# Kernel optimization log

Hardware: AMD Instinct MI355X
Metric: run time of the kernel (lower is better)

## Reference

```python
import jax, jax.numpy as jnp
import numpy as np

N = 8192
IN_CH = 256
OUT_CH = 64
LEAKY_ALPHA = 0.5
NEG_INF = -9e15  # -9000000000000000.0 from the source


def setup_inputs() -> dict:
    key = jax.random.key(0)
    k1, k2, k3, k4 = jax.random.split(key, 4)
    h = jax.random.normal(k1, (N, IN_CH), dtype=jnp.float32)
    adj = jax.random.randint(k2, (N, N), 0, 2, dtype=jnp.int32)
    # Xavier-uniform-style init for parameters
    limW = float(np.sqrt(6.0 / (IN_CH + OUT_CH)))
    W = jax.random.uniform(k3, (IN_CH, OUT_CH), dtype=jnp.float32, minval=-limW, maxval=limW)
    lima = float(np.sqrt(6.0 / (2 * OUT_CH + 1)))
    a = jax.random.uniform(k4, (2 * OUT_CH, 1), dtype=jnp.float32, minval=-lima, maxval=lima)
    return {"h": h, "adj": adj, "W": W, "a": a}


def reference(h, adj, W, a):
    # Wh: [N, out]
    Wh = h @ W
    # additive attention score: e[i,j] = leakyrelu(Wh[i]@a1 + Wh[j]@a2)
    Wh1 = Wh @ a[:OUT_CH]   # [N, 1]
    Wh2 = Wh @ a[OUT_CH:]   # [N, 1]
    e = Wh1 + Wh2.T         # [N, N]
    e = jnp.where(e >= 0, e, LEAKY_ALPHA * e)  # LeakyReLU(0.5)
    # adjacency masking + row softmax
    att = jnp.where(adj > 0, e, jnp.float32(NEG_INF))
    att = jax.nn.softmax(att, axis=1)
    # dropout is identity in eval mode (training=False)
    h_prime = att @ Wh      # [N, out]
    # concat=True branch applies ReLU on the output
    return jax.nn.relu(h_prime)
```

## Files before the change

### kernel.cpp

```cpp
#include <hip/hip_runtime.h>
#include <stdint.h>

#define NN 8192
#define INC 256
#define OUTC 64
#define LOG2E 1.4426950408889634f

typedef __bf16 bf16x8 __attribute__((ext_vector_type(8)));
typedef float f32x4 __attribute__((ext_vector_type(4)));

__device__ __forceinline__ unsigned short f2bf(float x) {
    union { float f; unsigned u; } v; v.f = x;
    unsigned u = v.u;
    u += 0x7fffu + ((u >> 16) & 1u);
    return (unsigned short)(u >> 16);
}

#if __has_builtin(__builtin_amdgcn_exp2f)
#define EXP2(x) __builtin_amdgcn_exp2f(x)
#else
#define EXP2(x) exp2f(x)
#endif

__global__ __launch_bounds__(256) void gat_k1(
        const float* __restrict__ h, const float* __restrict__ W,
        const float* __restrict__ a,
        unsigned short* __restrict__ WhTf, float* __restrict__ Wh1,
        float* __restrict__ Wh2) {
    __shared__ float Ws[256 * 65];
    __shared__ float hs[16 * INC];
    __shared__ float Wa1s[256], Wa2s[256], as_[128];
    __shared__ unsigned short wt[OUTC][16];
    const int r0 = blockIdx.x * 16;
    const int t  = threadIdx.x;
    if (t < 128) as_[t] = a[t];
    #pragma unroll
    for (int it = 0; it < 16; ++it) {
        int idx = it * 1024 + t * 4;
        float4 v = *reinterpret_cast<const float4*>(W + idx);
        int k = idx >> 6, c = idx & 63;
        float* dst = &Ws[k * 65 + c];
        dst[0] = v.x; dst[1] = v.y; dst[2] = v.z; dst[3] = v.w;
    }
    #pragma unroll
    for (int it = 0; it < 4; ++it) {
        int idx = it * 1024 + t * 4;
        float4 v = *reinterpret_cast<const float4*>(h + (size_t)r0 * INC + idx);
        hs[idx] = v.x; hs[idx + 1] = v.y; hs[idx + 2] = v.z; hs[idx + 3] = v.w;
    }
    __syncthreads();
    {
        float s1 = 0.f, s2 = 0.f;
        #pragma unroll 8
        for (int c = 0; c < OUTC; ++c) {
            float w = Ws[t * 65 + c];
            s1 = fmaf(w, as_[c], s1);
            s2 = fmaf(w, as_[OUTC + c], s2);
        }
        Wa1s[t] = s1; Wa2s[t] = s2;
    }
    __syncthreads();
    const int w = t >> 6, lane = t & 63;
    const int c = lane;
    const float* hr = &hs[w * 4 * INC];
    float acc0 = 0.f, acc1 = 0.f, acc2 = 0.f, acc3 = 0.f;
    #pragma unroll 8
    for (int k = 0; k < INC; ++k) {
        float wv = Ws[k * 65 + c];
        acc0 = fmaf(hr[k],           wv, acc0);
        acc1 = fmaf(hr[INC + k],     wv, acc1);
        acc2 = fmaf(hr[2 * INC + k], wv, acc2);
        acc3 = fmaf(hr[3 * INC + k], wv, acc3);
    }
    float s1r[4] = {0.f, 0.f, 0.f, 0.f}, s2r[4] = {0.f, 0.f, 0.f, 0.f};
    #pragma unroll
    for (int kk = 0; kk < 4; ++kk) {
        int k = kk * 64 + lane;
        float wa1v = Wa1s[k], wa2v = Wa2s[k];
        #pragma unroll
        for (int r = 0; r < 4; ++r) {
            float hv = hr[r * INC + k];
            s1r[r] = fmaf(hv, wa1v, s1r[r]);
            s2r[r] = fmaf(hv, wa2v, s2r[r]);
        }
    }
    #pragma unroll
    for (int r = 0; r < 4; ++r) {
        float s1 = s1r[r], s2 = s2r[r];
        #pragma unroll
        for (int off = 32; off; off >>= 1) {
            s1 += __shfl_xor(s1, off, 64);
            s2 += __shfl_xor(s2, off, 64);
        }
        if (lane == 0) { Wh1[r0 + w * 4 + r] = s1; Wh2[r0 + w * 4 + r] = s2; }
    }
    wt[c][w * 4 + 0] = f2bf(acc0);
    wt[c][w * 4 + 1] = f2bf(acc1);
    wt[c][w * 4 + 2] = f2bf(acc2);
    wt[c][w * 4 + 3] = f2bf(acc3);
    __syncthreads();
    if (t < 128) {
        int m = t & 15, ct = (t >> 4) & 3, oct = t >> 6;
        int Kb = r0 >> 5;
        int qh = (r0 >> 3) & 3;
        int lanef = (qh + oct) * 16 + m;
        int cidx = ct * 16 + m;
        ushort4 v0, v1;
        v0.x = wt[cidx][oct * 8 + 0]; v0.y = wt[cidx][oct * 8 + 1];
        v0.z = wt[cidx][oct * 8 + 2]; v0.w = wt[cidx][oct * 8 + 3];
        v1.x = wt[cidx][oct * 8 + 4]; v1.y = wt[cidx][oct * 8 + 5];
        v1.z = wt[cidx][oct * 8 + 6]; v1.w = wt[cidx][oct * 8 + 7];
        unsigned short* dst = WhTf + (((size_t)(Kb * 4 + ct)) << 9) + lanef * 8;
        *reinterpret_cast<ushort4*>(dst)     = v0;
        *reinterpret_cast<ushort4*>(dst + 4) = v1;
    }
}

__global__ void gat_k2(const float* __restrict__ Wh2, float* __restrict__ M) {
    __shared__ float red[16];
    int t = threadIdx.x;
    float4 v0 = *reinterpret_cast<const float4*>(Wh2 + t * 4);
    float4 v1 = *reinterpret_cast<const float4*>(Wh2 + 4096 + t * 4);
    float m = fmaxf(fmaxf(fmaxf(v0.x, v0.y), fmaxf(v0.z, v0.w)),
                    fmaxf(fmaxf(v1.x, v1.y), fmaxf(v1.z, v1.w)));
    #pragma unroll
    for (int off = 32; off; off >>= 1) m = fmaxf(m, __shfl_xor(m, off, 64));
    if ((t & 63) == 0) red[t >> 6] = m;
    __syncthreads();
    if (t == 0) {
        float mm = red[0];
        #pragma unroll
        for (int i = 1; i < 16; ++i) mm = fmaxf(mm, red[i]);
        *M = mm;
    }
}

__global__ __launch_bounds__(512, 4) void gat_k3(
        const int* __restrict__ adj, const unsigned short* __restrict__ WhTf,
        const float* __restrict__ Wh1, const float* __restrict__ Wh2,
        const float* __restrict__ Mp, float* __restrict__ out) {
    __shared__ float accs[8][16 * OUTC];
    __shared__ float wh2s[NN];
    __shared__ float ls[8][16];
    const int r0 = blockIdx.x * 16;
    const int t = threadIdx.x;
    const int w = t >> 6, lane = t & 63;
    const int m = lane & 15, q = lane >> 4;
    #pragma unroll
    for (int it = 0; it < 4; ++it) {
        int idx = it * 2048 + t * 4;
        float4 v = *reinterpret_cast<const float4*>(Wh2 + idx);
        wh2s[idx] = v.x; wh2s[idx + 1] = v.y; wh2s[idx + 2] = v.z; wh2s[idx + 3] = v.w;
    }
    const int row = r0 + m;
    const float wh1 = Wh1[row];
    const float Mv = *Mp;
    const float sM = wh1 + Mv;
    const float mhat = fmaxf(sM, 0.5f * sM);
    const float mh2 = mhat * LOG2E;
    const int* __restrict__ arow = adj + (size_t)row * NN;
    __syncthreads();
    f32x4 acc[4] = {{0,0,0,0},{0,0,0,0},{0,0,0,0},{0,0,0,0}};
    float lpart = 0.f;

    const int qo = q * 8;
    int jt = w;
    int4 a0 = *reinterpret_cast<const int4*>(arow + jt * 64 + qo);
    int4 a1 = *reinterpret_cast<const int4*>(arow + jt * 64 + qo + 4);
    int4 a2 = *reinterpret_cast<const int4*>(arow + jt * 64 + 32 + qo);
    int4 a3 = *reinterpret_cast<const int4*>(arow + jt * 64 + 32 + qo + 4);

    #pragma unroll 2
    for (int it = 0; it < 16; ++it, jt += 8) {
        const unsigned short* fb = WhTf + (size_t)jt * 4096 + lane * 8;
        bf16x8 bv0 = *reinterpret_cast<const bf16x8*>(fb);
        bf16x8 bv1 = *reinterpret_cast<const bf16x8*>(fb + 512);
        bf16x8 bv2 = *reinterpret_cast<const bf16x8*>(fb + 1024);
        bf16x8 bv3 = *reinterpret_cast<const bf16x8*>(fb + 1536);
        bf16x8 bv4 = *reinterpret_cast<const bf16x8*>(fb + 2048);
        bf16x8 bv5 = *reinterpret_cast<const bf16x8*>(fb + 2560);
        bf16x8 bv6 = *reinterpret_cast<const bf16x8*>(fb + 3072);
        bf16x8 bv7 = *reinterpret_cast<const bf16x8*>(fb + 3584);
        const int jn = (it < 15) ? jt + 8 : w;
        const int* __restrict__ anext = arow + jn * 64 + qo;
        int4 n0 = *reinterpret_cast<const int4*>(anext);
        int4 n1 = *reinterpret_cast<const int4*>(anext + 4);
        int4 n2 = *reinterpret_cast<const int4*>(anext + 32);
        int4 n3 = *reinterpret_cast<const int4*>(anext + 36);
        const int jb = jt * 64 + qo;
        float4 s0 = *reinterpret_cast<const float4*>(&wh2s[jb]);
        float4 s1 = *reinterpret_cast<const float4*>(&wh2s[jb + 4]);
        float4 s2 = *reinterpret_cast<const float4*>(&wh2s[jb + 32]);
        float4 s3 = *reinterpret_cast<const float4*>(&wh2s[jb + 36]);
        float sv[16] = {s0.x, s0.y, s0.z, s0.w, s1.x, s1.y, s1.z, s1.w,
                        s2.x, s2.y, s2.z, s2.w, s3.x, s3.y, s3.z, s3.w};
        int   av[16] = {a0.x, a0.y, a0.z, a0.w, a1.x, a1.y, a1.z, a1.w,
                        a2.x, a2.y, a2.z, a2.w, a3.x, a3.y, a3.z, a3.w};
        float p[16];
        #pragma unroll
        for (int e = 0; e < 16; ++e) {
            float s  = wh1 + sv[e];
            float lk = fmaxf(s, 0.5f * s);
            float ar = fmaf(lk, LOG2E, -mh2);
            float pe = EXP2(ar);
            p[e] = (av[e] > 0) ? pe : 0.f;
        }
        float lp = 0.f;
        #pragma unroll
        for (int e = 0; e < 16; ++e) lp += p[e];
        lpart += lp;
        bf16x8 af0, af1;
        #pragma unroll
        for (int e = 0; e < 8; ++e) { af0[e] = (__bf16)p[e]; af1[e] = (__bf16)p[8 + e]; }
        acc[0] = __builtin_amdgcn_mfma_f32_16x16x32_bf16(af0, bv0, acc[0], 0, 0, 0);
        acc[1] = __builtin_amdgcn_mfma_f32_16x16x32_bf16(af0, bv1, acc[1], 0, 0, 0);
        acc[2] = __builtin_amdgcn_mfma_f32_16x16x32_bf16(af0, bv2, acc[2], 0, 0, 0);
        acc[3] = __builtin_amdgcn_mfma_f32_16x16x32_bf16(af0, bv3, acc[3], 0, 0, 0);
        acc[0] = __builtin_amdgcn_mfma_f32_16x16x32_bf16(af1, bv4, acc[0], 0, 0, 0);
        acc[1] = __builtin_amdgcn_mfma_f32_16x16x32_bf16(af1, bv5, acc[1], 0, 0, 0);
        acc[2] = __builtin_amdgcn_mfma_f32_16x16x32_bf16(af1, bv6, acc[2], 0, 0, 0);
        acc[3] = __builtin_amdgcn_mfma_f32_16x16x32_bf16(af1, bv7, acc[3], 0, 0, 0);
        a0 = n0; a1 = n1; a2 = n2; a3 = n3;
    }
    #pragma unroll
    for (int ct = 0; ct < 4; ++ct)
        #pragma unroll
        for (int r = 0; r < 4; ++r)
            accs[w][(q * 4 + r) * OUTC + ct * 16 + m] = acc[ct][r];
    float l = lpart;
    l += __shfl_xor(l, 16, 64);
    l += __shfl_xor(l, 32, 64);
    if (lane < 16) ls[w][lane] = l;
    __syncthreads();
    for (int e = t; e < 16 * OUTC; e += 512) {
        int rr = e >> 6, cc = e & 63;
        float s = 0.f;
        #pragma unroll
        for (int ww = 0; ww < 8; ++ww) s += accs[ww][e];
        float lsum = 0.f;
        #pragma unroll
        for (int ww = 0; ww < 8; ++ww) lsum += ls[ww][rr];
        float o = s / lsum;
        out[(size_t)(r0 + rr) * OUTC + cc] = o > 0.f ? o : 0.f;
    }
}

extern "C" void kernel_launch(void* const* d_in, const int* in_sizes, int n_in,
                              void* d_out, int out_size, void* d_ws, size_t ws_size,
                              hipStream_t stream) {
    const float* h   = (const float*)d_in[0];
    const int*   adj = (const int*)d_in[1];
    const float* W   = (const float*)d_in[2];
    const float* a   = (const float*)d_in[3];
    float* out = (float*)d_out;

    char* base = (char*)d_ws;
    float* Wh1 = (float*)(base);
    float* Wh2 = (float*)(base + 32768);
    float* Mp  = (float*)(base + 65536);
    unsigned short* WhTf = (unsigned short*)(base + 69632);

    gat_k1<<<NN / 16, 256, 0, stream>>>(h, W, a, WhTf, Wh1, Wh2);
    gat_k2<<<1, 1024, 0, stream>>>(Wh2, Mp);
    gat_k3<<<NN / 16, 512, 0, stream>>>(adj, WhTf, Wh1, Wh2, Mp, out);
}
```

Baseline: 398.3 us.

## Shrink attention block to four waves, drop LDS Wh2 staging, deepen adj prefetch

The attention-aggregation kernel now runs 256 threads per block instead of 512. Each wave steps through 32-column chunks (one set of four MFMAs per step) rather than 64-column chunks. The 32KB shared-memory copy of Wh2 and its barrier are removed, and Wh2 is read straight from global memory. The adjacency loads now use a two-stage register prefetch. The aim is lower per-block LDS and register pressure, which should allow more resident blocks and better hiding of the adjacency-stream latency. The cost is more loop iterations, repeated global/L1 reads of Wh2, and a fixed output reduction across only four waves.

```diff
diff --git a/kernel.cpp b/kernel.cpp
--- a/kernel.cpp
+++ b/kernel.cpp
@@ -135,23 +135,17 @@
     }
 }
 
-__global__ __launch_bounds__(512, 4) void gat_k3(
+__global__ __launch_bounds__(256, 5) void gat_k3(
         const int* __restrict__ adj, const unsigned short* __restrict__ WhTf,
         const float* __restrict__ Wh1, const float* __restrict__ Wh2,
         const float* __restrict__ Mp, float* __restrict__ out) {
-    __shared__ float accs[8][16 * OUTC];
-    __shared__ float wh2s[NN];
-    __shared__ float ls[8][16];
+    __shared__ float accs[4][16 * OUTC];
+    __shared__ float ls[4][16];
     const int r0 = blockIdx.x * 16;
     const int t = threadIdx.x;
     const int w = t >> 6, lane = t & 63;
     const int m = lane & 15, q = lane >> 4;
-    #pragma unroll
-    for (int it = 0; it < 4; ++it) {
-        int idx = it * 2048 + t * 4;
-        float4 v = *reinterpret_cast<const float4*>(Wh2 + idx);
-        wh2s[idx] = v.x; wh2s[idx + 1] = v.y; wh2s[idx + 2] = v.z; wh2s[idx + 3] = v.w;
-    }
+    const int qo = q * 8;
     const int row = r0 + m;
     const float wh1 = Wh1[row];
     const float Mv = *Mp;
@@ -159,68 +153,49 @@
     const float mhat = fmaxf(sM, 0.5f * sM);
     const float mh2 = mhat * LOG2E;
     const int* __restrict__ arow = adj + (size_t)row * NN;
-    __syncthreads();
     f32x4 acc[4] = {{0,0,0,0},{0,0,0,0},{0,0,0,0},{0,0,0,0}};
     float lpart = 0.f;
 
-    const int qo = q * 8;
-    int jt = w;
-    int4 a0 = *reinterpret_cast<const int4*>(arow + jt * 64 + qo);
-    int4 a1 = *reinterpret_cast<const int4*>(arow + jt * 64 + qo + 4);
-    int4 a2 = *reinterpret_cast<const int4*>(arow + jt * 64 + 32 + qo);
-    int4 a3 = *reinterpret_cast<const int4*>(arow + jt * 64 + 32 + qo + 4);
+    int4 c0 = *reinterpret_cast<const int4*>(arow + (size_t)w * 32 + qo);
+    int4 c1 = *reinterpret_cast<const int4*>(arow + (size_t)w * 32 + qo + 4);
+    int4 d0 = *reinterpret_cast<const int4*>(arow + (size_t)(w + 4) * 32 + qo);
+    int4 d1 = *reinterpret_cast<const int4*>(arow + (size_t)(w + 4) * 32 + qo + 4);
 
     #pragma unroll 2
-    for (int it = 0; it < 16; ++it, jt += 8) {
-        const unsigned short* fb = WhTf + (size_t)jt * 4096 + lane * 8;
+    for (int i = 0; i < 64; ++i) {
+        const int jt = w + i * 4;
+        const unsigned short* fb = WhTf + (size_t)jt * 2048 + lane * 8;
         bf16x8 bv0 = *reinterpret_cast<const bf16x8*>(fb);
         bf16x8 bv1 = *reinterpret_cast<const bf16x8*>(fb + 512);
         bf16x8 bv2 = *reinterpret_cast<const bf16x8*>(fb + 1024);
         bf16x8 bv3 = *reinterpret_cast<const bf16x8*>(fb + 1536);
-        bf16x8 bv4 = *reinterpret_cast<const bf16x8*>(fb + 2048);
-        bf16x8 bv5 = *reinterpret_cast<const bf16x8*>(fb + 2560);
-        bf16x8 bv6 = *reinterpret_cast<const bf16x8*>(fb + 3072);
-        bf16x8 bv7 = *reinterpret_cast<const bf16x8*>(fb + 3584);
-        const int jn = (it < 15) ? jt + 8 : w;
-        const int* __restrict__ anext = arow + jn * 64 + qo;
-        int4 n0 = *reinterpret_cast<const int4*>(anext);
-        int4 n1 = *reinterpret_cast<const int4*>(anext + 4);
-        int4 n2 = *reinterpret_cast<const int4*>(anext + 32);
-        int4 n3 = *reinterpret_cast<const int4*>(anext + 36);
-        const int jb = jt * 64 + qo;
-        float4 s0 = *reinterpret_cast<const float4*>(&wh2s[jb]);
-        float4 s1 = *reinterpret_cast<const float4*>(&wh2s[jb + 4]);
-        float4 s2 = *reinterpret_cast<const float4*>(&wh2s[jb + 32]);
-        float4 s3 = *reinterpret_cast<const float4*>(&wh2s[jb + 36]);
-        float sv[16] = {s0.x, s0.y, s0.z, s0.w, s1.x, s1.y, s1.z, s1.w,
-                        s2.x, s2.y, s2.z, s2.w, s3.x, s3.y, s3.z, s3.w};
-        int   av[16] = {a0.x, a0.y, a0.z, a0.w, a1.x, a1.y, a1.z, a1.w,
-                        a2.x, a2.y, a2.z, a2.w, a3.x, a3.y, a3.z, a3.w};
-        float p[16];
-        #pragma unroll
-        for (int e = 0; e < 16; ++e) {
+        const int jb = jt * 32 + qo;
+        float4 s0 = *reinterpret_cast<const float4*>(Wh2 + jb);
+        float4 s1 = *reinterpret_cast<const float4*>(Wh2 + jb + 4);
+        const int jn = (i < 62) ? (jt + 8) : w;
+        const int* __restrict__ an = arow + (size_t)jn * 32 + qo;
+        int4 e0 = *reinterpret_cast<const int4*>(an);
+        int4 e1 = *reinterpret_cast<const int4*>(an + 4);
+        float sv[8] = {s0.x, s0.y, s0.z, s0.w, s1.x, s1.y, s1.z, s1.w};
+        int   av[8] = {c0.x, c0.y, c0.z, c0.w, c1.x, c1.y, c1.z, c1.w};
+        float p[8];
+        #pragma unroll
+        for (int e = 0; e < 8; ++e) {
             float s  = wh1 + sv[e];
             float lk = fmaxf(s, 0.5f * s);
             float ar = fmaf(lk, LOG2E, -mh2);
             float pe = EXP2(ar);
             p[e] = (av[e] > 0) ? pe : 0.f;
         }
-        float lp = 0.f;
-        #pragma unroll
-        for (int e = 0; e < 16; ++e) lp += p[e];
-        lpart += lp;
-        bf16x8 af0, af1;
-        #pragma unroll
-        for (int e = 0; e < 8; ++e) { af0[e] = (__bf16)p[e]; af1[e] = (__bf16)p[8 + e]; }
-        acc[0] = __builtin_amdgcn_mfma_f32_16x16x32_bf16(af0, bv0, acc[0], 0, 0, 0);
-        acc[1] = __builtin_amdgcn_mfma_f32_16x16x32_bf16(af0, bv1, acc[1], 0, 0, 0);
-        acc[2] = __builtin_amdgcn_mfma_f32_16x16x32_bf16(af0, bv2, acc[2], 0, 0, 0);
-        acc[3] = __builtin_amdgcn_mfma_f32_16x16x32_bf16(af0, bv3, acc[3], 0, 0, 0);
-        acc[0] = __builtin_amdgcn_mfma_f32_16x16x32_bf16(af1, bv4, acc[0], 0, 0, 0);
-        acc[1] = __builtin_amdgcn_mfma_f32_16x16x32_bf16(af1, bv5, acc[1], 0, 0, 0);
-        acc[2] = __builtin_amdgcn_mfma_f32_16x16x32_bf16(af1, bv6, acc[2], 0, 0, 0);
-        acc[3] = __builtin_amdgcn_mfma_f32_16x16x32_bf16(af1, bv7, acc[3], 0, 0, 0);
-        a0 = n0; a1 = n1; a2 = n2; a3 = n3;
+        lpart += ((p[0] + p[1]) + (p[2] + p[3])) + ((p[4] + p[5]) + (p[6] + p[7]));
+        bf16x8 af;
+        #pragma unroll
+        for (int e = 0; e < 8; ++e) af[e] = (__bf16)p[e];
+        acc[0] = __builtin_amdgcn_mfma_f32_16x16x32_bf16(af, bv0, acc[0], 0, 0, 0);
+        acc[1] = __builtin_amdgcn_mfma_f32_16x16x32_bf16(af, bv1, acc[1], 0, 0, 0);
+        acc[2] = __builtin_amdgcn_mfma_f32_16x16x32_bf16(af, bv2, acc[2], 0, 0, 0);
+        acc[3] = __builtin_amdgcn_mfma_f32_16x16x32_bf16(af, bv3, acc[3], 0, 0, 0);
+        c0 = d0; c1 = d1; d0 = e0; d1 = e1;
     }
     #pragma unroll
     for (int ct = 0; ct < 4; ++ct)
@@ -232,14 +207,11 @@
     l += __shfl_xor(l, 32, 64);
     if (lane < 16) ls[w][lane] = l;
     __syncthreads();
-    for (int e = t; e < 16 * OUTC; e += 512) {
+    #pragma unroll
+    for (int e = t; e < 16 * OUTC; e += 256) {
         int rr = e >> 6, cc = e & 63;
-        float s = 0.f;
-        #pragma unroll
-        for (int ww = 0; ww < 8; ++ww) s += accs[ww][e];
-        float lsum = 0.f;
-        #pragma unroll
-        for (int ww = 0; ww < 8; ++ww) lsum += ls[ww][rr];
+        float s = (accs[0][e] + accs[1][e]) + (accs[2][e] + accs[3][e]);
+        float lsum = (ls[0][rr] + ls[1][rr]) + (ls[2][rr] + ls[3][rr]);
         float o = s / lsum;
         out[(size_t)(r0 + rr) * OUTC + cc] = o > 0.f ? o : 0.f;
     }
@@ -262,5 +234,5 @@
 
     gat_k1<<<NN / 16, 256, 0, stream>>>(h, W, a, WhTf, Wh1, Wh2);
     gat_k2<<<1, 1024, 0, stream>>>(Wh2, Mp);
-    gat_k3<<<NN / 16, 512, 0, stream>>>(adj, WhTf, Wh1, Wh2, Mp, out);
-}
+    gat_k3<<<NN / 16, 256, 0, stream>>>(adj, WhTf, Wh1, Wh2, Mp, out);
+}
```

Measured after the change: 481.0 us. 20.8% more time.
